# Kernel tuning notes

Measured on AMD Instinct MI355X. Metric: run time of the kernel, lower is better.

## Reference

```python
import jax, jax.numpy as jnp
import numpy as np


def setup_inputs() -> dict:
    key = jax.random.key(0)
    k1, k2 = jax.random.split(key)
    B, L, T, H = 8, 12, 1024, 256
    h_blth = jax.random.normal(k1, (B, L, T, H), dtype=jnp.float32)
    attn_w = jax.random.normal(k2, (1, H), dtype=jnp.float32) * (1.0 / np.sqrt(H))
    attn_b = jnp.zeros((1,), dtype=jnp.float32)
    return {"h_blth": h_blth, "attn_w": attn_w, "attn_b": attn_b}


def reference(h_blth, attn_w, attn_b):
    # s = Linear(H -> 1)(h).squeeze(-1): [B, L, T]
    s = jnp.einsum('blth,oh->blt', h_blth, attn_w) + attn_b[0]
    # global (non-causal) max over time axis, as in the original code
    s_max = jnp.max(s, axis=2, keepdims=True)
    exp_s = jnp.exp(s - s_max)                      # [B, L, T]
    cum_exp = jnp.cumsum(exp_s, axis=2)             # [B, L, T]
    weighted_h = exp_s[..., None] * h_blth          # [B, L, T, H]
    cum_weighted_h = jnp.cumsum(weighted_h, axis=2) # [B, L, T, H]
    ctx = cum_weighted_h / (cum_exp[..., None] + 1e-12)
    return h_blth + ctx
```

## Files before the change

### kernel.cpp

```cpp
#include <hip/hip_runtime.h>

#define RWS 96
#define TT  1024
#define HH  256
#define CT  64
#define NC  (TT/CT)

__global__ __launch_bounds__(256) void k1_scores(
    const float* __restrict__ h, const float* __restrict__ attn_w,
    const float* __restrict__ attn_b, float* __restrict__ e_g,
    float* __restrict__ W_g) {
  const int blk  = blockIdx.x;
  const int row  = blk / NC;
  const int c    = blk % NC;
  const int t0   = c * CT;
  const int tid  = threadIdx.x;
  const int lane = tid & 63;
  const int wave = tid >> 6;

  const float4 wv  = reinterpret_cast<const float4*>(attn_w)[lane];
  const float bias = attn_b[0];
  const float* hrow = h + (size_t)row * TT * HH;

  float4 acc = make_float4(0.f, 0.f, 0.f, 0.f);

  for (int tt = wave; tt < CT; tt += 4) {
    const int t = t0 + tt;
    const float4 hv =
        reinterpret_cast<const float4*>(hrow + (size_t)t * HH)[lane];
    float p = hv.x * wv.x + hv.y * wv.y + hv.z * wv.z + hv.w * wv.w;
#pragma unroll
    for (int off = 32; off; off >>= 1) p += __shfl_xor(p, off);
    const float e = __expf(p + bias);
    if (lane == 0) e_g[(size_t)row * TT + t] = e;
    acc.x = fmaf(e, hv.x, acc.x);
    acc.y = fmaf(e, hv.y, acc.y);
    acc.z = fmaf(e, hv.z, acc.z);
    acc.w = fmaf(e, hv.w, acc.w);
  }

  __shared__ float wlds[4][HH];
  reinterpret_cast<float4*>(wlds[wave])[lane] = acc;
  __syncthreads();
  const float wsum = wlds[0][tid] + wlds[1][tid] + wlds[2][tid] + wlds[3][tid];
  W_g[((size_t)row * NC + c) * HH + tid] = wsum;
}

__global__ __launch_bounds__(256) void k3_out(
    const float* __restrict__ h, const float* __restrict__ e_g,
    const float* __restrict__ W_g, float* __restrict__ out) {
  const int blk  = blockIdx.x;
  const int row  = blk >> 2;
  const int q    = blk & 3;
  const int tid  = threadIdx.x;
  const int lane = tid & 63;
  const int wave = tid >> 6;

  __shared__ float e_lds[TT];
  reinterpret_cast<float4*>(e_lds)[tid] =
      reinterpret_cast<const float4*>(e_g + (size_t)row * TT)[tid];
  __syncthreads();

  const int ts = q * 256 + wave * CT;

  float ex = 0.f;
  for (int i = lane; i < ts; i += 64) ex += e_lds[i];
#pragma unroll
  for (int off = 32; off; off >>= 1) ex += __shfl_xor(ex, off);

  float4 run = make_float4(0.f, 0.f, 0.f, 0.f);
  const int ncc = ts / CT;
  const float4* Wp = reinterpret_cast<const float4*>(W_g + (size_t)row * NC * HH) + lane;
  for (int cc = 0; cc < ncc; ++cc) {
    const float4 wv = Wp[(size_t)cc * (HH / 4)];
    run.x += wv.x; run.y += wv.y; run.z += wv.z; run.w += wv.w;
  }

  const float4* hp =
      reinterpret_cast<const float4*>(h + ((size_t)row * TT + ts) * HH) + lane;
  float4* op =
      reinterpret_cast<float4*>(out + ((size_t)row * TT + ts) * HH) + lane;
  float cum = ex;
#pragma unroll 4
  for (int tt = 0; tt < CT; ++tt) {
    const float e = e_lds[ts + tt];
    cum += e;
    const float ic = 1.f / (cum + 1e-12f);
    const float4 hv = hp[(size_t)tt * (HH / 4)];
    run.x = fmaf(e, hv.x, run.x);
    run.y = fmaf(e, hv.y, run.y);
    run.z = fmaf(e, hv.z, run.z);
    run.w = fmaf(e, hv.w, run.w);
    float4 o;
    o.x = fmaf(run.x, ic, hv.x);
    o.y = fmaf(run.y, ic, hv.y);
    o.z = fmaf(run.z, ic, hv.z);
    o.w = fmaf(run.w, ic, hv.w);
    op[(size_t)tt * (HH / 4)] = o;
  }
}

extern "C" void kernel_launch(void* const* d_in, const int* in_sizes, int n_in,
                              void* d_out, int out_size, void* d_ws,
                              size_t ws_size, hipStream_t stream) {
  const float* h      = (const float*)d_in[0];
  const float* attn_w = (const float*)d_in[1];
  const float* attn_b = (const float*)d_in[2];
  float* out = (float*)d_out;

  float* e_g = (float*)d_ws;
  float* W_g = e_g + (size_t)RWS * TT;

  k1_scores<<<RWS * NC, 256, 0, stream>>>(h, attn_w, attn_b, e_g, W_g);
  k3_out<<<RWS * 4, 256, 0, stream>>>(h, e_g, W_g, out);
}
```

Baseline: 54.40 us.

## Split output pass into single-wave blocks with shuffle-broadcast scores and nontemporal IO

The second kernel now launches one 64-thread block per (row, 64-step chunk) instead of four-wave blocks covering a quarter row. The LDS staging and barrier go away: each lane loads one score and the value is broadcast with a wave shuffle. It also uses the hardware reciprocal instead of a divide, nontemporal loads and stores for the streaming h/out traffic, and a deeper unroll. This trades more, smaller blocks and redundant prefix reads of scores and chunk sums for better scheduling flexibility and less cache pollution. The approximate reciprocal may slightly change numerics.

```diff
diff --git a/kernel.cpp b/kernel.cpp
--- a/kernel.cpp
+++ b/kernel.cpp
@@ -6,7 +6,9 @@
 #define CT  64
 #define NC  (TT/CT)
 
-__global__ __launch_bounds__(256) void k1_scores(
+typedef float f32x4 __attribute__((ext_vector_type(4)));
+
+__global__ __launch_bounds__(256) void ta_pass1(
     const float* __restrict__ h, const float* __restrict__ attn_w,
     const float* __restrict__ attn_b, float* __restrict__ e_g,
     float* __restrict__ W_g) {
@@ -46,57 +48,53 @@
   W_g[((size_t)row * NC + c) * HH + tid] = wsum;
 }
 
-__global__ __launch_bounds__(256) void k3_out(
+__global__ __launch_bounds__(64) void ta_pass2(
     const float* __restrict__ h, const float* __restrict__ e_g,
     const float* __restrict__ W_g, float* __restrict__ out) {
   const int blk  = blockIdx.x;
-  const int row  = blk >> 2;
-  const int q    = blk & 3;
-  const int tid  = threadIdx.x;
-  const int lane = tid & 63;
-  const int wave = tid >> 6;
+  const int row  = blk >> 4;
+  const int c    = blk & (NC - 1);
+  const int ts   = c * CT;
+  const int lane = threadIdx.x;
 
-  __shared__ float e_lds[TT];
-  reinterpret_cast<float4*>(e_lds)[tid] =
-      reinterpret_cast<const float4*>(e_g + (size_t)row * TT)[tid];
-  __syncthreads();
-
-  const int ts = q * 256 + wave * CT;
+  const float* er = e_g + (size_t)row * TT;
+  const float ev = er[ts + lane];
 
   float ex = 0.f;
-  for (int i = lane; i < ts; i += 64) ex += e_lds[i];
+  for (int i = lane; i < ts; i += 64) ex += er[i];
 #pragma unroll
   for (int off = 32; off; off >>= 1) ex += __shfl_xor(ex, off);
 
   float4 run = make_float4(0.f, 0.f, 0.f, 0.f);
-  const int ncc = ts / CT;
-  const float4* Wp = reinterpret_cast<const float4*>(W_g + (size_t)row * NC * HH) + lane;
-  for (int cc = 0; cc < ncc; ++cc) {
+  const float4* Wp =
+      reinterpret_cast<const float4*>(W_g + (size_t)row * NC * HH) + lane;
+  for (int cc = 0; cc < c; ++cc) {
     const float4 wv = Wp[(size_t)cc * (HH / 4)];
     run.x += wv.x; run.y += wv.y; run.z += wv.z; run.w += wv.w;
   }
 
-  const float4* hp =
-      reinterpret_cast<const float4*>(h + ((size_t)row * TT + ts) * HH) + lane;
-  float4* op =
-      reinterpret_cast<float4*>(out + ((size_t)row * TT + ts) * HH) + lane;
+  const f32x4* hp =
+      reinterpret_cast<const f32x4*>(h + ((size_t)row * TT + ts) * HH) + lane;
+  f32x4* op =
+      reinterpret_cast<f32x4*>(out + ((size_t)row * TT + ts) * HH) + lane;
+
   float cum = ex;
-#pragma unroll 4
+#pragma unroll 8
   for (int tt = 0; tt < CT; ++tt) {
-    const float e = e_lds[ts + tt];
+    const float e = __shfl(ev, tt);
     cum += e;
-    const float ic = 1.f / (cum + 1e-12f);
-    const float4 hv = hp[(size_t)tt * (HH / 4)];
+    const float ic = __builtin_amdgcn_rcpf(cum + 1e-12f);
+    const f32x4 hv = __builtin_nontemporal_load(hp + (size_t)tt * (HH / 4));
     run.x = fmaf(e, hv.x, run.x);
     run.y = fmaf(e, hv.y, run.y);
     run.z = fmaf(e, hv.z, run.z);
     run.w = fmaf(e, hv.w, run.w);
-    float4 o;
+    f32x4 o;
     o.x = fmaf(run.x, ic, hv.x);
     o.y = fmaf(run.y, ic, hv.y);
     o.z = fmaf(run.z, ic, hv.z);
     o.w = fmaf(run.w, ic, hv.w);
-    op[(size_t)tt * (HH / 4)] = o;
+    __builtin_nontemporal_store(o, op + (size_t)tt * (HH / 4));
   }
 }
 
@@ -111,6 +109,6 @@
   float* e_g = (float*)d_ws;
   float* W_g = e_g + (size_t)RWS * TT;
 
-  k1_scores<<<RWS * NC, 256, 0, stream>>>(h, attn_w, attn_b, e_g, W_g);
-  k3_out<<<RWS * 4, 256, 0, stream>>>(h, e_g, W_g, out);
+  ta_pass1<<<RWS * NC, 256, 0, stream>>>(h, attn_w, attn_b, e_g, W_g);
+  ta_pass2<<<RWS * NC, 64, 0, stream>>>(h, e_g, W_g, out);
 }
```

Measured after the change: 56.71 us. +4.3%, slower.
